# Performance work log

Measured on AMD Instinct MI355X. Metric: run time of the kernel, lower is better.

## Reference

```python
import jax, jax.numpy as jnp
import numpy as np

L, B, E, H = 2048, 2, 1024, 16
HD = E // H


def setup_inputs() -> dict:
    key = jax.random.key(0)
    ks = jax.random.split(key, 7)
    return {
        "query": jax.random.normal(ks[0], (L, B, E), dtype=jnp.float32),
        "key": jax.random.normal(ks[1], (L, B, E), dtype=jnp.float32),
        "value": jax.random.normal(ks[2], (L, B, E), dtype=jnp.float32),
        "in_proj_weight": jax.random.normal(ks[3], (3 * E, E), dtype=jnp.float32) * 0.02,
        "in_proj_bias": jax.random.normal(ks[4], (3 * E,), dtype=jnp.float32) * 0.02,
        "out_proj_weight": jax.random.normal(ks[5], (E, E), dtype=jnp.float32) * 0.02,
        "out_proj_bias": jax.random.normal(ks[6], (E,), dtype=jnp.float32) * 0.02,
    }


def reference(query, key, value, in_proj_weight, in_proj_bias, out_proj_weight, out_proj_bias):
    l, b, e = query.shape
    scaling = jnp.asarray(HD, query.dtype) ** -0.5
    wq, wk, wv = jnp.split(in_proj_weight, 3, axis=0)
    bq, bk, bv = jnp.split(in_proj_bias, 3)
    q = (query @ wq.T + bq) * scaling          # [L,B,E]
    k = key @ wk.T + bk
    v = value @ wv.T + bv

    def to_heads(t):  # [L,B,E] -> [B*H, L, HD]
        return t.reshape(l, b * H, HD).transpose(1, 0, 2)

    q, k, v = to_heads(q), to_heads(k), to_heads(v)
    scores = jnp.einsum('nld,nmd->nlm', q, k)  # [B*H, L, L] materialized as in legacy MHA
    attn = jax.nn.softmax(scores, axis=-1)
    out = jnp.einsum('nlm,nmd->nld', attn, v)  # [B*H, L, HD]
    out = out.transpose(1, 0, 2).reshape(l, b, e)
    return out @ out_proj_weight.T + out_proj_bias
```

## Files before the change

kernel.cpp:

```cpp
#include <hip/hip_runtime.h>
#include <hip/hip_bf16.h>

typedef __attribute__((ext_vector_type(8))) short short8;
typedef __attribute__((ext_vector_type(4))) float floatx4;
typedef __attribute__((ext_vector_type(16))) float floatx16;

#define L_SEQ 2048
#define EMB   1024
#define HD    64
#define QSCALE 0.18033688011112042f
#define FIXMAX2 11.541560327111707f

__device__ __forceinline__ unsigned short f2bf(float f) {
    unsigned int u = __float_as_uint(f);
    u += 0x7fffu + ((u >> 16) & 1u);
    return (unsigned short)(u >> 16);
}
__device__ __forceinline__ unsigned pkbf(float a, float b) {
    return (unsigned)f2bf(a) | ((unsigned)f2bf(b) << 16);
}
__device__ __forceinline__ unsigned pkbf2(float a, float b) {
    __hip_bfloat162 h = __float22bfloat162_rn(make_float2(a, b));
    unsigned u; __builtin_memcpy(&u, &h, 4); return u;
}
__device__ __forceinline__ void gld_lds16(const void* g, void* l) {
    __builtin_amdgcn_global_load_lds(
        (const __attribute__((address_space(1))) unsigned*)g,
        (__attribute__((address_space(3))) unsigned*)l, 16, 0, 0);
}
__device__ __forceinline__ float fexp2(float x) {
    return __builtin_amdgcn_exp2f(x);
}

__global__ __launch_bounds__(256) void convert_all(
    const float* __restrict__ q, const float* __restrict__ k,
    const float* __restrict__ v, const float* __restrict__ ipw,
    const float* __restrict__ opw,
    unsigned short* __restrict__ Abq, unsigned short* __restrict__ Abk,
    unsigned short* __restrict__ Abv, unsigned short* __restrict__ Wipb,
    unsigned short* __restrict__ Wopb)
{
    const int NA = 1048576, NIP = 786432;
    int idx = blockIdx.x * 256 + threadIdx.x;
    const float* src; unsigned short* dst; int o;
    if (idx < NA)            { src = q;   dst = Abq;  o = idx; }
    else if (idx < 2 * NA)   { src = k;   dst = Abk;  o = idx - NA; }
    else if (idx < 3 * NA)   { src = v;   dst = Abv;  o = idx - 2 * NA; }
    else if (idx < 3 * NA + NIP) { src = ipw; dst = Wipb; o = idx - 3 * NA; }
    else                     { src = opw; dst = Wopb; o = idx - 3 * NA - NIP; }
    float4 f = ((const float4*)src)[o];
    ((uint2*)dst)[o] = make_uint2(pkbf(f.x, f.y), pkbf(f.z, f.w));
}

__global__ __launch_bounds__(256, 3) void qkv_gemm(
    const unsigned short* __restrict__ Abq, const unsigned short* __restrict__ Abk,
    const unsigned short* __restrict__ Abv, const unsigned short* __restrict__ Wb,
    const float* __restrict__ Bip,
    unsigned short* __restrict__ Qf, unsigned short* __restrict__ Kf,
    unsigned short* __restrict__ Vf)
{
    __shared__ unsigned short lds[17408];
    unsigned short* As = lds;
    unsigned short* Bs = lds + 8192;

    const int tid = threadIdx.x, lane = tid & 63, w = tid >> 6;
    const int wm = (w & 1) * 64, wn = (w >> 1) * 64;
    const int m0 = blockIdx.x * 128, n0 = blockIdx.y * 128;
    const int cn = lane & 15, g = lane >> 4;
    const int z = n0 >> 10;
    const unsigned short* Ag = (z == 0) ? Abq : (z == 1) ? Abk : Abv;

    floatx4 acc[4][4];
    #pragma unroll
    for (int i = 0; i < 4; ++i)
        #pragma unroll
        for (int j = 0; j < 4; ++j) acc[i][j] = (floatx4){0.f, 0.f, 0.f, 0.f};

    for (int k0 = 0; k0 < EMB; k0 += 64) {
        __syncthreads();
        #pragma unroll
        for (int p = 0; p < 4; ++p) {
            int u0 = (p * 4 + w) * 64, u = u0 + lane, row = u >> 3, sl = u & 7;
            gld_lds16(Ag + (size_t)(m0 + row) * EMB + k0 + ((sl ^ (row & 7)) * 8), &As[u0 * 8]);
            gld_lds16(Wb + (size_t)(n0 + row) * EMB + k0 + ((sl ^ (row & 7)) * 8), &Bs[u0 * 8]);
        }
        __syncthreads();
        #pragma unroll
        for (int kc = 0; kc < 2; ++kc) {
            short8 a4[4], b4[4];
            #pragma unroll
            for (int i = 0; i < 4; ++i)
                a4[i] = *(const short8*)&As[(wm + i * 16 + cn) * 64 + (((kc * 4 + g) ^ (cn & 7)) * 8)];
            #pragma unroll
            for (int j = 0; j < 4; ++j)
                b4[j] = *(const short8*)&Bs[(wn + j * 16 + cn) * 64 + (((kc * 4 + g) ^ (cn & 7)) * 8)];
            #pragma unroll
            for (int i = 0; i < 4; ++i)
                #pragma unroll
                for (int j = 0; j < 4; ++j)
                    acc[i][j] = __builtin_amdgcn_mfma_f32_16x16x32_bf16(a4[i], b4[j], acc[i][j], 0, 0, 0);
        }
    }

    const int c32l = lane & 31, hi5 = lane >> 5;
    const int b = w >> 1, hl = w & 1;

    if (z < 2) {
        __syncthreads();
        #pragma unroll
        for (int j = 0; j < 4; ++j) {
            int cl = wn + j * 16 + cn;
            float bv = Bip[n0 + cl];
            #pragma unroll
            for (int i = 0; i < 4; ++i)
                #pragma unroll
                for (int r = 0; r < 4; ++r) {
                    int rr = wm + i * 16 + g * 4 + r;
                    float vv = acc[i][j][r] + bv;
                    lds[rr * 136 + cl] = f2bf(z == 0 ? vv * QSCALE : vv);
                }
        }
        __syncthreads();
        const int h0 = (n0 & 1023) >> 6;
        const int nn = b * 16 + h0 + hl;
        unsigned short* Dst = (z == 0) ? Qf : Kf;
        #pragma unroll
        for (int cc = 0; cc < 8; ++cc) {
            int t32l = cc >> 2, kk = cc & 3;
            int rr = (t32l * 32 + c32l) * 2 + b;
            int ccol = hl * 64 + kk * 16 + hi5 * 8;
            uint4 val = *(const uint4*)&lds[rr * 136 + ccol];
            int ck = (nn * 64 + (m0 >> 6) + t32l) * 4 + kk;
            *(uint4*)(Dst + (size_t)ck * 512 + lane * 8) = val;
        }
    } else {
        __syncthreads();
        #pragma unroll
        for (int j = 0; j < 4; ++j) {
            int col_l = wn + j * 16 + cn;
            float bv = Bip[n0 + col_l];
            #pragma unroll
            for (int i = 0; i < 4; ++i) {
                int rrb = wm + i * 16 + g * 4;
                int l0 = rrb >> 1;
                float v0 = acc[i][j][0] + bv, v1 = acc[i][j][1] + bv;
                float v2 = acc[i][j][2] + bv, v3 = acc[i][j][3] + bv;
                *(unsigned*)&lds[col_l * 136 +      l0] = pkbf(v0, v2);
                *(unsigned*)&lds[col_l * 136 + 64 + l0] = pkbf(v1, v3);
            }
        }
        __syncthreads();
        const int h0 = (n0 - 2048) >> 6;
        const int nn = b * 16 + h0 + hl;
        #pragma unroll
        for (int cc = 0; cc < 8; ++cc) {
            int dt = cc >> 2, kk2l = cc & 3;
            int col_l = hl * 64 + dt * 32 + c32l;
            int keyl = kk2l * 16 + hi5 * 8;
            uint4 val = *(const uint4*)&lds[col_l * 136 + b * 64 + keyl];
            int cv = nn * 256 + ((m0 >> 5) + kk2l) * 2 + dt;
            *(uint4*)(Vf + (size_t)cv * 512 + lane * 8) = val;
        }
    }
}

__global__ __launch_bounds__(256, 2) void flash_attn_k(
    const unsigned short* __restrict__ Qf, const unsigned short* __restrict__ Kf,
    const unsigned short* __restrict__ Vf, unsigned short* __restrict__ Oh)
{
    const int id = blockIdx.y * 32 + blockIdx.x;
    const int xcd = id & 7, slot = id >> 3;
    const int n = xcd * 4 + (slot & 3);
    const int q0 = (slot >> 2) * 64;

    __shared__ float Uf[64 * 67];

    const int tid = threadIdx.x, lane = tid & 63, w = tid >> 6;
    const int c32 = lane & 31, hi = lane >> 5;

    short8 qf[2][4];
    #pragma unroll
    for (int qt = 0; qt < 2; ++qt)
        #pragma unroll
        for (int kk = 0; kk < 4; ++kk)
            qf[qt][kk] = *(const short8*)(Qf + ((size_t)((n * 64 + (q0 >> 5) + qt) * 4 + kk)) * 512 + lane * 8);

    floatx16 acc_o[2][2];
    #pragma unroll
    for (int qt = 0; qt < 2; ++qt)
        #pragma unroll
        for (int dt = 0; dt < 2; ++dt)
            #pragma unroll
            for (int r = 0; r < 16; ++r) acc_o[qt][dt][r] = 0.f;
    float lsum0 = 0.f, lsum1 = 0.f;

    const unsigned short* kbase = Kf + ((size_t)n * 256 + w * 64) * 512 + lane * 8;
    const unsigned short* vbase = Vf + ((size_t)n * 256 + w * 64) * 512 + lane * 8;

#define FLOAD(KF, VF, T) do {                                               \
    const unsigned short* _kp = kbase + (size_t)(T) * 2048;                 \
    const unsigned short* _vp = vbase + (size_t)(T) * 2048;                 \
    _Pragma("unroll")                                                       \
    for (int kk = 0; kk < 4; ++kk)                                          \
        KF[kk] = *(const short8*)(_kp + kk * 512);                          \
    _Pragma("unroll")                                                       \
    for (int kc = 0; kc < 2; ++kc)                                          \
        _Pragma("unroll")                                                   \
        for (int dt = 0; dt < 2; ++dt)                                      \
            VF[kc][dt] = *(const short8*)(_vp + (kc * 2 + dt) * 512);       \
} while (0)

#define FCOMP(KF, VF) do {                                                  \
    floatx16 s_[2];                                                         \
    _Pragma("unroll")                                                       \
    for (int qt = 0; qt < 2; ++qt) {                                        \
        _Pragma("unroll")                                                   \
        for (int r = 0; r < 16; ++r) s_[qt][r] = -FIXMAX2;                  \
        __builtin_amdgcn_s_setprio(1);                                      \
        _Pragma("unroll")                                                   \
        for (int kk = 0; kk < 4; ++kk)                                      \
            s_[qt] = __builtin_amdgcn_mfma_f32_32x32x16_bf16(KF[kk], qf[qt][kk], s_[qt], 0, 0, 0); \
        __builtin_amdgcn_s_setprio(0);                                      \
    }                                                                       \
    _Pragma("unroll")                                                       \
    for (int qt = 0; qt < 2; ++qt) {                                        \
        float p_[16];                                                       \
        _Pragma("unroll")                                                   \
        for (int r = 0; r < 16; ++r) p_[r] = fexp2(s_[qt][r]);              \
        float ls_ = ((p_[0] + p_[1]) + (p_[2] + p_[3])) + ((p_[4] + p_[5]) + (p_[6] + p_[7])) \
                  + ((p_[8] + p_[9]) + (p_[10] + p_[11])) + ((p_[12] + p_[13]) + (p_[14] + p_[15])); \
        if (qt == 0) lsum0 += ls_; else lsum1 += ls_;                       \
        short8 pa_[2];                                                      \
        _Pragma("unroll")                                                   \
        for (int kc = 0; kc < 2; ++kc) {                                    \
            unsigned A_ = pkbf2(p_[kc * 8 + 0], p_[kc * 8 + 1]);            \
            unsigned B_ = pkbf2(p_[kc * 8 + 2], p_[kc * 8 + 3]);            \
            unsigned C_ = pkbf2(p_[kc * 8 + 4], p_[kc * 8 + 5]);            \
            unsigned D_ = pkbf2(p_[kc * 8 + 6], p_[kc * 8 + 7]);            \
            asm("v_permlane32_swap_b32 %0, %1" : "+v"(A_), "+v"(C_));       \
            asm("v_permlane32_swap_b32 %0, %1" : "+v"(B_), "+v"(D_));       \
            union { unsigned u[4]; short8 v; } cv_;                         \
            cv_.u[0] = A_; cv_.u[1] = B_; cv_.u[2] = C_; cv_.u[3] = D_;     \
            pa_[kc] = cv_.v;                                                \
        }                                                                   \
        __builtin_amdgcn_s_setprio(1);                                      \
        _Pragma("unroll")                                                   \
        for (int kc = 0; kc < 2; ++kc)                                      \
            _Pragma("unroll")                                               \
            for (int dt = 0; dt < 2; ++dt)                                  \
                acc_o[qt][dt] = __builtin_amdgcn_mfma_f32_32x32x16_bf16(pa_[kc], VF[kc][dt], acc_o[qt][dt], 0, 0, 0); \
        __builtin_amdgcn_s_setprio(0);                                      \
    }                                                                       \
} while (0)

    short8 kfA[4], vfA[2][2], kfB[4], vfB[2][2];
    FLOAD(kfA, vfA, 0);
    for (int t = 0; t < 16; t += 2) {
        FLOAD(kfB, vfB, t + 1);
        FCOMP(kfA, vfA);
        if (t + 2 < 16) FLOAD(kfA, vfA, t + 2);
        FCOMP(kfB, vfB);
    }
#undef FLOAD
#undef FCOMP

    {
        float a0 = lsum0, b0 = lsum0;
        asm("v_permlane32_swap_b32 %0, %1" : "+v"(a0), "+v"(b0));
        lsum0 = a0 + b0;
        float a1 = lsum1, b1 = lsum1;
        asm("v_permlane32_swap_b32 %0, %1" : "+v"(a1), "+v"(b1));
        lsum1 = a1 + b1;
    }

#define BLOB_STORE() do {                                                  \
    _Pragma("unroll")                                                      \
    for (int qt = 0; qt < 2; ++qt)                                         \
        _Pragma("unroll")                                                  \
        for (int dt = 0; dt < 2; ++dt)                                     \
            _Pragma("unroll")                                              \
            for (int r = 0; r < 16; ++r)                                   \
                Uf[ub + (qt * 2 + dt) * 16 + r] = acc_o[qt][dt][r];        \
    Uf[ub + 64] = lsum0; Uf[ub + 65] = lsum1;                              \
} while (0)
#define BLOB_ADD() do {                                                    \
    _Pragma("unroll")                                                      \
    for (int qt = 0; qt < 2; ++qt)                                         \
        _Pragma("unroll")                                                  \
        for (int dt = 0; dt < 2; ++dt)                                     \
            _Pragma("unroll")                                              \
            for (int r = 0; r < 16; ++r)                                   \
                acc_o[qt][dt][r] += Uf[ub + (qt * 2 + dt) * 16 + r];       \
    lsum0 += Uf[ub + 64]; lsum1 += Uf[ub + 65];                            \
} while (0)

    const int ub = lane * 67;
    __syncthreads();
    if (w == 3) BLOB_STORE();
    __syncthreads();
    if (w == 2) { BLOB_ADD(); BLOB_STORE(); }
    __syncthreads();
    if (w == 1) { BLOB_ADD(); BLOB_STORE(); }
    __syncthreads();
    if (w == 0) {
        BLOB_ADD();
        float inv0 = 1.0f / lsum0, inv1 = 1.0f / lsum1;
        const int hib = hi * 16;
        const int bb = n >> 4, h = n & 15;
        #pragma unroll
        for (int qt = 0; qt < 2; ++qt) {
            float invq = qt ? inv1 : inv0;
            #pragma unroll
            for (int r = 0; r < 16; ++r) {
                int idx = ((r & 3) + 8 * (r >> 2)) * 4 + hib;
                float invr = __int_as_float(__builtin_amdgcn_ds_bpermute(idx, __float_as_int(invq)));
                int q = q0 + qt * 32 + (r & 3) + 8 * (r >> 2) + hi * 4;
                #pragma unroll
                for (int dt = 0; dt < 2; ++dt) {
                    int e = h * 64 + dt * 32 + c32;
                    Oh[((size_t)q * 2 + bb) * EMB + e] = f2bf(acc_o[qt][dt][r] * invr);
                }
            }
        }
    }
#undef BLOB_STORE
#undef BLOB_ADD
}

__global__ __launch_bounds__(256, 4) void out_gemm(
    const unsigned short* __restrict__ Oh, const unsigned short* __restrict__ Wob,
    const float* __restrict__ bo, float* __restrict__ out)
{
    __shared__ unsigned short As[64 * 64];
    __shared__ unsigned short Bs[128 * 64];

    const int tid = threadIdx.x, lane = tid & 63, w = tid >> 6;
    const int wm = (w & 1) * 32, wn = (w >> 1) * 64;
    const int m0 = blockIdx.x * 64, n0 = blockIdx.y * 128;
    const int cn = lane & 15, g = lane >> 4;

    floatx4 acc[2][4];
    #pragma unroll
    for (int i = 0; i < 2; ++i)
        #pragma unroll
        for (int j = 0; j < 4; ++j) acc[i][j] = (floatx4){0.f, 0.f, 0.f, 0.f};

    for (int k0 = 0; k0 < EMB; k0 += 64) {
        __syncthreads();
        #pragma unroll
        for (int p = 0; p < 4; ++p) {
            int u0 = (p * 4 + w) * 64, u = u0 + lane, row = u >> 3, sl = u & 7;
            if (p < 2)
                gld_lds16(Oh + (size_t)(m0 + row) * EMB + k0 + ((sl ^ (row & 7)) * 8), &As[u0 * 8]);
            gld_lds16(Wob + (size_t)(n0 + row) * EMB + k0 + ((sl ^ (row & 7)) * 8), &Bs[u0 * 8]);
        }
        __syncthreads();
        #pragma unroll
        for (int kc = 0; kc < 2; ++kc) {
            short8 a4[2], b4[4];
            #pragma unroll
            for (int i = 0; i < 2; ++i)
                a4[i] = *(const short8*)&As[(wm + i * 16 + cn) * 64 + (((kc * 4 + g) ^ (cn & 7)) * 8)];
            #pragma unroll
            for (int j = 0; j < 4; ++j)
                b4[j] = *(const short8*)&Bs[(wn + j * 16 + cn) * 64 + (((kc * 4 + g) ^ (cn & 7)) * 8)];
            #pragma unroll
            for (int i = 0; i < 2; ++i)
                #pragma unroll
                for (int j = 0; j < 4; ++j)
                    acc[i][j] = __builtin_amdgcn_mfma_f32_16x16x32_bf16(a4[i], b4[j], acc[i][j], 0, 0, 0);
        }
    }

    #pragma unroll
    for (int j = 0; j < 4; ++j) {
        int col = n0 + wn + j * 16 + cn;
        float bv = bo[col];
        #pragma unroll
        for (int i = 0; i < 2; ++i)
            #pragma unroll
            for (int r = 0; r < 4; ++r)
                out[(size_t)(m0 + wm + i * 16 + g * 4 + r) * EMB + col] = acc[i][j][r] + bv;
    }
}

extern "C" void kernel_launch(void* const* d_in, const int* in_sizes, int n_in,
                              void* d_out, int out_size, void* d_ws, size_t ws_size,
                              hipStream_t stream) {
    const float* q   = (const float*)d_in[0];
    const float* k   = (const float*)d_in[1];
    const float* v   = (const float*)d_in[2];
    const float* ipw = (const float*)d_in[3];
    const float* ipb = (const float*)d_in[4];
    const float* opw = (const float*)d_in[5];
    const float* opb = (const float*)d_in[6];
    float* out = (float*)d_out;

    const size_t HE = (size_t)32 * L_SEQ * HD;
    unsigned short* Qf   = (unsigned short*)d_ws;
    unsigned short* Kf   = Qf + HE;
    unsigned short* Vf   = Kf + HE;
    unsigned short* Wipb = Vf + HE;
    unsigned short* Wopb = Wipb + (size_t)3 * EMB * EMB;
    unsigned short* Abq  = Wopb + (size_t)EMB * EMB;
    unsigned short* Abk  = Abq + HE;
    unsigned short* Abv  = Abk + HE;
    unsigned short* Oh   = Abq;

    convert_all<<<dim3(16384), 256, 0, stream>>>(q, k, v, ipw, opw, Abq, Abk, Abv, Wipb, Wopb);
    qkv_gemm<<<dim3(32, 24), 256, 0, stream>>>(Abq, Abk, Abv, Wipb, ipb, Qf, Kf, Vf);
    flash_attn_k<<<dim3(32, 32), 256, 0, stream>>>(Qf, Kf, Vf, Oh);
    out_gemm<<<dim3(64, 8), 256, 0, stream>>>(Oh, Wopb, opb, out);
}
```

Baseline: 200.8 us.

## Widen conversion, swizzle GEMM blocks per XCD, tree-reduce attention, smaller out tiles

The conversion kernel now handles 8 floats per thread and emits 16-byte stores, so it launches half as many threads. qkv_gemm and out_gemm remap block IDs so that neighbouring M tiles land on the same XCD, which is meant to improve L2 reuse. out_gemm also shrinks its tile to 64x64 with twice as many blocks, giving more parallelism at the cost of less reuse per block. The flash attention cross-wave reduction changes from a three-step serial chain to a two-level tree using double LDS scratch, and the K/V pointers now advance incrementally in a non-unrolled loop.

Measured after the change: 203.2 us. About the same (+1.2%).

```diff
diff --git a/kernel.cpp b/kernel.cpp
--- a/kernel.cpp
+++ b/kernel.cpp
@@ -40,16 +40,20 @@
     unsigned short* __restrict__ Abv, unsigned short* __restrict__ Wipb,
     unsigned short* __restrict__ Wopb)
 {
-    const int NA = 1048576, NIP = 786432;
+    const int NA2 = 524288, NIP2 = 393216;
     int idx = blockIdx.x * 256 + threadIdx.x;
     const float* src; unsigned short* dst; int o;
-    if (idx < NA)            { src = q;   dst = Abq;  o = idx; }
-    else if (idx < 2 * NA)   { src = k;   dst = Abk;  o = idx - NA; }
-    else if (idx < 3 * NA)   { src = v;   dst = Abv;  o = idx - 2 * NA; }
-    else if (idx < 3 * NA + NIP) { src = ipw; dst = Wipb; o = idx - 3 * NA; }
-    else                     { src = opw; dst = Wopb; o = idx - 3 * NA - NIP; }
-    float4 f = ((const float4*)src)[o];
-    ((uint2*)dst)[o] = make_uint2(pkbf(f.x, f.y), pkbf(f.z, f.w));
+    if (idx < NA2)            { src = q;   dst = Abq;  o = idx; }
+    else if (idx < 2 * NA2)   { src = k;   dst = Abk;  o = idx - NA2; }
+    else if (idx < 3 * NA2)   { src = v;   dst = Abv;  o = idx - 2 * NA2; }
+    else if (idx < 3 * NA2 + NIP2) { src = ipw; dst = Wipb; o = idx - 3 * NA2; }
+    else                      { src = opw; dst = Wopb; o = idx - 3 * NA2 - NIP2; }
+    float4 f0 = ((const float4*)src)[o * 2];
+    float4 f1 = ((const float4*)src)[o * 2 + 1];
+    uint4 r;
+    r.x = pkbf(f0.x, f0.y); r.y = pkbf(f0.z, f0.w);
+    r.z = pkbf(f1.x, f1.y); r.w = pkbf(f1.z, f1.w);
+    ((uint4*)dst)[o] = r;
 }
 
 __global__ __launch_bounds__(256, 3) void qkv_gemm(
@@ -65,7 +69,10 @@
 
     const int tid = threadIdx.x, lane = tid & 63, w = tid >> 6;
     const int wm = (w & 1) * 64, wn = (w >> 1) * 64;
-    const int m0 = blockIdx.x * 128, n0 = blockIdx.y * 128;
+    const int id = blockIdx.y * 32 + blockIdx.x;
+    const int xcd = id & 7, s = id >> 3;
+    const int m0 = (xcd * 4 + (s & 3)) * 128;
+    const int n0 = (s >> 2) * 128;
     const int cn = lane & 15, g = lane >> 4;
     const int z = n0 >> 10;
     const unsigned short* Ag = (z == 0) ? Abq : (z == 1) ? Abk : Abv;
@@ -173,7 +180,7 @@
     const int n = xcd * 4 + (slot & 3);
     const int q0 = (slot >> 2) * 64;
 
-    __shared__ float Uf[64 * 67];
+    __shared__ float Uf[2 * 64 * 67];
 
     const int tid = threadIdx.x, lane = tid & 63, w = tid >> 6;
     const int c32 = lane & 31, hi = lane >> 5;
@@ -194,20 +201,19 @@
             for (int r = 0; r < 16; ++r) acc_o[qt][dt][r] = 0.f;
     float lsum0 = 0.f, lsum1 = 0.f;
 
-    const unsigned short* kbase = Kf + ((size_t)n * 256 + w * 64) * 512 + lane * 8;
-    const unsigned short* vbase = Vf + ((size_t)n * 256 + w * 64) * 512 + lane * 8;
-
-#define FLOAD(KF, VF, T) do {                                               \
-    const unsigned short* _kp = kbase + (size_t)(T) * 2048;                 \
-    const unsigned short* _vp = vbase + (size_t)(T) * 2048;                 \
+    const unsigned short* kp = Kf + ((size_t)n * 256 + w * 64) * 512 + lane * 8;
+    const unsigned short* vp = Vf + ((size_t)n * 256 + w * 64) * 512 + lane * 8;
+
+#define FLOAD(KF, VF) do {                                                  \
     _Pragma("unroll")                                                       \
     for (int kk = 0; kk < 4; ++kk)                                          \
-        KF[kk] = *(const short8*)(_kp + kk * 512);                          \
+        KF[kk] = *(const short8*)(kp + kk * 512);                           \
     _Pragma("unroll")                                                       \
     for (int kc = 0; kc < 2; ++kc)                                          \
         _Pragma("unroll")                                                   \
         for (int dt = 0; dt < 2; ++dt)                                      \
-            VF[kc][dt] = *(const short8*)(_vp + (kc * 2 + dt) * 512);       \
+            VF[kc][dt] = *(const short8*)(vp + (kc * 2 + dt) * 512);        \
+    kp += 2048; vp += 2048;                                                 \
 } while (0)
 
 #define FCOMP(KF, VF) do {                                                  \
@@ -254,11 +260,12 @@
 } while (0)
 
     short8 kfA[4], vfA[2][2], kfB[4], vfB[2][2];
-    FLOAD(kfA, vfA, 0);
+    FLOAD(kfA, vfA);
+    #pragma unroll 1
     for (int t = 0; t < 16; t += 2) {
-        FLOAD(kfB, vfB, t + 1);
+        FLOAD(kfB, vfB);
         FCOMP(kfA, vfA);
-        if (t + 2 < 16) FLOAD(kfA, vfA, t + 2);
+        if (t + 2 < 16) FLOAD(kfA, vfA);
         FCOMP(kfB, vfB);
     }
 #undef FLOAD
@@ -273,37 +280,37 @@
         lsum1 = a1 + b1;
     }
 
-#define BLOB_STORE() do {                                                  \
+#define BLOB_STORE(base) do {                                              \
     _Pragma("unroll")                                                      \
     for (int qt = 0; qt < 2; ++qt)                                         \
         _Pragma("unroll")                                                  \
         for (int dt = 0; dt < 2; ++dt)                                     \
             _Pragma("unroll")                                              \
             for (int r = 0; r < 16; ++r)                                   \
-                Uf[ub + (qt * 2 + dt) * 16 + r] = acc_o[qt][dt][r];        \
-    Uf[ub + 64] = lsum0; Uf[ub + 65] = lsum1;                              \
+                Uf[(base) + (qt * 2 + dt) * 16 + r] = acc_o[qt][dt][r];    \
+    Uf[(base) + 64] = lsum0; Uf[(base) + 65] = lsum1;                      \
 } while (0)
-#define BLOB_ADD() do {                                                    \
+#define BLOB_ADD(base) do {                                                \
     _Pragma("unroll")                                                      \
     for (int qt = 0; qt < 2; ++qt)                                         \
         _Pragma("unroll")                                                  \
         for (int dt = 0; dt < 2; ++dt)                                     \
             _Pragma("unroll")                                              \
             for (int r = 0; r < 16; ++r)                                   \
-                acc_o[qt][dt][r] += Uf[ub + (qt * 2 + dt) * 16 + r];       \
-    lsum0 += Uf[ub + 64]; lsum1 += Uf[ub + 65];                            \
+                acc_o[qt][dt][r] += Uf[(base) + (qt * 2 + dt) * 16 + r];   \
+    lsum0 += Uf[(base) + 64]; lsum1 += Uf[(base) + 65];                    \
 } while (0)
 
-    const int ub = lane * 67;
+    const int r0 = lane * 67, r1 = 64 * 67 + lane * 67;
     __syncthreads();
-    if (w == 3) BLOB_STORE();
+    if (w == 1) BLOB_STORE(r0);
+    if (w == 3) BLOB_STORE(r1);
     __syncthreads();
-    if (w == 2) { BLOB_ADD(); BLOB_STORE(); }
-    __syncthreads();
-    if (w == 1) { BLOB_ADD(); BLOB_STORE(); }
+    if (w == 0) BLOB_ADD(r0);
+    if (w == 2) { BLOB_ADD(r1); BLOB_STORE(r1); }
     __syncthreads();
     if (w == 0) {
-        BLOB_ADD();
+        BLOB_ADD(r1);
         float inv0 = 1.0f / lsum0, inv1 = 1.0f / lsum1;
         const int hib = hi * 16;
         const int bb = n >> 4, h = n & 15;
@@ -332,48 +339,50 @@
     const float* __restrict__ bo, float* __restrict__ out)
 {
     __shared__ unsigned short As[64 * 64];
-    __shared__ unsigned short Bs[128 * 64];
+    __shared__ unsigned short Bs[64 * 64];
 
     const int tid = threadIdx.x, lane = tid & 63, w = tid >> 6;
-    const int wm = (w & 1) * 32, wn = (w >> 1) * 64;
-    const int m0 = blockIdx.x * 64, n0 = blockIdx.y * 128;
+    const int wm = (w & 1) * 32, wn = (w >> 1) * 32;
+    const int id = blockIdx.y * 64 + blockIdx.x;
+    const int xcd = id & 7, slot = id >> 3;
+    const int m0 = (xcd * 8 + (slot & 7)) * 64;
+    const int n0 = (slot >> 3) * 64;
     const int cn = lane & 15, g = lane >> 4;
 
-    floatx4 acc[2][4];
+    floatx4 acc[2][2];
     #pragma unroll
     for (int i = 0; i < 2; ++i)
         #pragma unroll
-        for (int j = 0; j < 4; ++j) acc[i][j] = (floatx4){0.f, 0.f, 0.f, 0.f};
+        for (int j = 0; j < 2; ++j) acc[i][j] = (floatx4){0.f, 0.f, 0.f, 0.f};
 
     for (int k0 = 0; k0 < EMB; k0 += 64) {
         __syncthreads();
         #pragma unroll
-        for (int p = 0; p < 4; ++p) {
+        for (int p = 0; p < 2; ++p) {
             int u0 = (p * 4 + w) * 64, u = u0 + lane, row = u >> 3, sl = u & 7;
-            if (p < 2)
-                gld_lds16(Oh + (size_t)(m0 + row) * EMB + k0 + ((sl ^ (row & 7)) * 8), &As[u0 * 8]);
+            gld_lds16(Oh  + (size_t)(m0 + row) * EMB + k0 + ((sl ^ (row & 7)) * 8), &As[u0 * 8]);
             gld_lds16(Wob + (size_t)(n0 + row) * EMB + k0 + ((sl ^ (row & 7)) * 8), &Bs[u0 * 8]);
         }
         __syncthreads();
         #pragma unroll
         for (int kc = 0; kc < 2; ++kc) {
-            short8 a4[2], b4[4];
+            short8 a4[2], b4[2];
             #pragma unroll
             for (int i = 0; i < 2; ++i)
                 a4[i] = *(const short8*)&As[(wm + i * 16 + cn) * 64 + (((kc * 4 + g) ^ (cn & 7)) * 8)];
             #pragma unroll
-            for (int j = 0; j < 4; ++j)
+            for (int j = 0; j < 2; ++j)
                 b4[j] = *(const short8*)&Bs[(wn + j * 16 + cn) * 64 + (((kc * 4 + g) ^ (cn & 7)) * 8)];
             #pragma unroll
             for (int i = 0; i < 2; ++i)
                 #pragma unroll
-                for (int j = 0; j < 4; ++j)
+                for (int j = 0; j < 2; ++j)
                     acc[i][j] = __builtin_amdgcn_mfma_f32_16x16x32_bf16(a4[i], b4[j], acc[i][j], 0, 0, 0);
         }
     }
 
     #pragma unroll
-    for (int j = 0; j < 4; ++j) {
+    for (int j = 0; j < 2; ++j) {
         int col = n0 + wn + j * 16 + cn;
         float bv = bo[col];
         #pragma unroll
@@ -407,8 +416,8 @@
     unsigned short* Abv  = Abk + HE;
     unsigned short* Oh   = Abq;
 
-    convert_all<<<dim3(16384), 256, 0, stream>>>(q, k, v, ipw, opw, Abq, Abk, Abv, Wipb, Wopb);
+    convert_all<<<dim3(8192), 256, 0, stream>>>(q, k, v, ipw, opw, Abq, Abk, Abv, Wipb, Wopb);
     qkv_gemm<<<dim3(32, 24), 256, 0, stream>>>(Abq, Abk, Abv, Wipb, ipb, Qf, Kf, Vf);
     flash_attn_k<<<dim3(32, 32), 256, 0, stream>>>(Qf, Kf, Vf, Oh);
-    out_gemm<<<dim3(64, 8), 256, 0, stream>>>(Oh, Wopb, opb, out);
-}
+    out_gemm<<<dim3(64, 16), 256, 0, stream>>>(Oh, Wopb, opb, out);
+}
```
